# Kernel tuning notes

Hardware: AMD Instinct MI355X
Metric: run time of the kernel (lower is better)

Reference implementation:

```python
import jax, jax.numpy as jnp
import numpy as np

B, D, H, W = 32, 256, 32, 32
K = 1024
BETA = 0.25


def setup_inputs() -> dict:
    key = jax.random.key(0)
    k1, k2 = jax.random.split(key)
    z_e = jax.random.normal(k1, (B, D, H, W), dtype=jnp.float32)
    codebook_weight = jax.random.normal(k2, (K, D), dtype=jnp.float32)
    return {"z_e": z_e, "codebook_weight": codebook_weight}


def reference(z_e, codebook_weight):
    # NCHW -> NHWC, flatten to tokens [N, D]
    z_perm = jnp.transpose(z_e, (0, 2, 3, 1))            # [B, H, W, D]
    z_flat = z_perm.reshape(-1, codebook_weight.shape[1])  # [N, D]

    # Squared Euclidean distances (argmin-equivalent to torch.cdist argmin)
    # d2[n, k] = ||z_n||^2 - 2 z_n . c_k + ||c_k||^2
    d2 = (jnp.sum(z_flat * z_flat, axis=1, keepdims=True)
          - 2.0 * (z_flat @ codebook_weight.T)
          + jnp.sum(codebook_weight * codebook_weight, axis=1)[None, :])  # [N, K]
    codebook_idx = jnp.argmin(d2, axis=1)                 # [N]

    # one-hot @ codebook == gather
    z_quant = codebook_weight[codebook_idx].reshape(z_perm.shape)  # [B,H,W,D]

    # straight-through estimator, back to NCHW
    z_q = z_perm + jax.lax.stop_gradient(z_quant - z_perm)
    z_q = jnp.transpose(z_q, (0, 3, 1, 2))                # [B, D, H, W]

    loss_codebook = jnp.mean((z_quant - jax.lax.stop_gradient(z_perm)) ** 2)
    loss_commit = jnp.mean((jax.lax.stop_gradient(z_quant) - z_perm) ** 2)
    loss_vq = loss_codebook + loss_commit * BETA

    return z_q, codebook_idx[:, None], loss_vq
```

## Files before the change

### kernel.cpp

```cpp
#include <hip/hip_runtime.h>
#include <hip/hip_bf16.h>
#include <cstdint>

#define B_ 32
#define D_ 256
#define K_ 1024
#define N_TOK 32768
#define Z_ELEMS 8388608
#define OUT_IDX_OFF Z_ELEMS
#define OUT_LOSS_OFF (Z_ELEMS + N_TOK)

#define WS_CNORM_OFF 0
#define WS_PART_OFF  4096
#define WS_CBF_OFF   8192
#define WS_TOP2_OFF  532480

#define MARGIN 1.25f

typedef __attribute__((ext_vector_type(8))) short short8v;
typedef __attribute__((ext_vector_type(4))) float f32x4;
typedef unsigned long long u64;

__device__ __forceinline__ unsigned short f2bf(float x) {
    unsigned u = __float_as_uint(x);
    return (unsigned short)((u + 0x7fffu + ((u >> 16) & 1u)) >> 16);
}
__device__ __forceinline__ unsigned packf(float f) {
    unsigned u = __float_as_uint(f);
    return (u & 0x80000000u) ? ~u : (u | 0x80000000u);
}
__device__ __forceinline__ float unpackf(unsigned p) {
    unsigned u = (p & 0x80000000u) ? (p & 0x7fffffffu) : ~p;
    return __uint_as_float(u);
}

__global__ __launch_bounds__(256)
void prep_kernel(const float* __restrict__ cb, float* __restrict__ cnorm,
                 unsigned char* __restrict__ cbf) {
    const int t = threadIdx.x;
    const int blk = blockIdx.x;
    {
        int k = blk * 64 + (t >> 2);
        int part = t & 3;
        const float4* row = reinterpret_cast<const float4*>(cb + k * D_);
        float s = 0.f;
#pragma unroll
        for (int j = 0; j < 16; ++j) {
            float4 v = row[part * 16 + j];
            s += v.x * v.x + v.y * v.y + v.z * v.z + v.w * v.w;
        }
        s += __shfl_xor(s, 1);
        s += __shfl_xor(s, 2);
        if (part == 0) cnorm[k] = s;
    }
#pragma unroll
    for (int w = 0; w < 8; ++w) {
        int g = blk * 2048 + w * 256 + t;
        int lane = g & 63, ct = (g >> 6) & 7, kc = (g >> 9) & 7, cblk = g >> 12;
        int code = cblk * 128 + ct * 16 + (lane & 15);
        int d0 = kc * 32 + (lane >> 4) * 8;
        const float* src = cb + code * 256 + d0;
        float4 a = *reinterpret_cast<const float4*>(src);
        float4 b2 = *reinterpret_cast<const float4*>(src + 4);
        uint4 pk;
        pk.x = (unsigned)f2bf(a.x) | ((unsigned)f2bf(a.y) << 16);
        pk.y = (unsigned)f2bf(a.z) | ((unsigned)f2bf(a.w) << 16);
        pk.z = (unsigned)f2bf(b2.x) | ((unsigned)f2bf(b2.y) << 16);
        pk.w = (unsigned)f2bf(b2.z) | ((unsigned)f2bf(b2.w) << 16);
        *reinterpret_cast<uint4*>(cbf + (size_t)g * 16) = pk;
    }
}

__global__ __launch_bounds__(256, 2)
void screen_kernel(const float* __restrict__ z, const unsigned char* __restrict__ cbf,
                   const float* __restrict__ cnorm, unsigned* __restrict__ top2) {
    __shared__ __align__(16) unsigned char zfB[32768];
    __shared__ float cns[1024];

    const int t = threadIdx.x;
    const int lane = t & 63;
    const int wv = t >> 6;
    const int blk = blockIdx.x;
    const int b = blk >> 4;
    const int hw0 = (blk & 15) << 6;
    const float* zb = z + ((size_t)b << 18) + hw0;

    for (int i = t; i < 1024; i += 256) cns[i] = cnorm[i];

    {
        const int stok = t & 63;
        const int sh = t >> 6;
        const int tt = stok >> 4;
#pragma unroll
        for (int uu = 0; uu < 8; ++uu) {
            int u = uu * 4 + sh;
            int d0 = u * 8;
            float v[8];
#pragma unroll
            for (int j = 0; j < 8; ++j) v[j] = zb[(size_t)(d0 + j) * 1024 + stok];
            uint4 pk;
            pk.x = (unsigned)f2bf(v[0]) | ((unsigned)f2bf(v[1]) << 16);
            pk.y = (unsigned)f2bf(v[2]) | ((unsigned)f2bf(v[3]) << 16);
            pk.z = (unsigned)f2bf(v[4]) | ((unsigned)f2bf(v[5]) << 16);
            pk.w = (unsigned)f2bf(v[6]) | ((unsigned)f2bf(v[7]) << 16);
            int slot = ((u & 3) << 4) | (stok & 15);
            *reinterpret_cast<uint4*>(zfB + tt * 8192 + (u >> 2) * 1024 + slot * 16) = pk;
        }
    }
    __syncthreads();

    const unsigned char* zrd = zfB + wv * 8192 + lane * 16;
    const int rbase = (lane >> 4) << 2;

    for (int cblk = 0; cblk < 8; ++cblk) {
        f32x4 acc[8];
#pragma unroll
        for (int mt = 0; mt < 8; ++mt) acc[mt] = (f32x4){0.f, 0.f, 0.f, 0.f};
        const unsigned char* abase = cbf + (size_t)cblk * 65536 + lane * 16;
#pragma unroll
        for (int kc = 0; kc < 8; ++kc) {
            short8v bfv = *reinterpret_cast<const short8v*>(zrd + kc * 1024);
#pragma unroll
            for (int mt = 0; mt < 8; ++mt) {
                short8v af = *reinterpret_cast<const short8v*>(abase + (kc * 8 + mt) * 1024);
                acc[mt] = __builtin_amdgcn_mfma_f32_16x16x32_bf16(af, bfv, acc[mt], 0, 0, 0);
            }
        }
        unsigned k1 = 0xFFFFFFFFu, k2 = 0xFFFFFFFFu;
#pragma unroll
        for (int mt = 0; mt < 8; ++mt) {
#pragma unroll
            for (int r = 0; r < 4; ++r) {
                int code = cblk * 128 + mt * 16 + rbase + r;
                float d2a = fmaf(-2.0f, acc[mt][r], cns[code]);
                unsigned key = (packf(d2a) & 0xFFFFFC00u) | (unsigned)code;
                if (key < k1) { k2 = k1; k1 = key; }
                else if (key < k2) { k2 = key; }
            }
        }
#pragma unroll
        for (int x = 16; x <= 32; x <<= 1) {
            unsigned o1 = __shfl_xor(k1, x);
            unsigned o2 = __shfl_xor(k2, x);
            unsigned n1, n2;
            if (k1 < o1) { n1 = k1; n2 = (k2 < o1) ? k2 : o1; }
            else         { n1 = o1; n2 = (o2 < k1) ? o2 : k1; }
            k1 = n1; k2 = n2;
        }
        if (lane < 16) {
            int token = blk * 64 + wv * 16 + lane;
            *reinterpret_cast<uint2*>(top2 + ((size_t)cblk * N_TOK + token) * 2) =
                make_uint2(k1, k2);
        }
    }
}

__global__ __launch_bounds__(256)
void refgather_kernel(const float* __restrict__ z, const float* __restrict__ cb,
                      const float* __restrict__ cnorm, const unsigned* __restrict__ top2,
                      float* __restrict__ out, float* __restrict__ partials) {
    __shared__ float zsm[32][261];
    __shared__ float crows[32][257];
    __shared__ int cand[32][16];
    __shared__ int cnt[32];
    __shared__ u64 bestk[32];
    __shared__ int sidx[32];
    __shared__ float red[256];
    __shared__ int maxc;

    const int t = threadIdx.x;
    const int bh = blockIdx.x;
    const int b = bh >> 5, h = bh & 31;
    const int n0 = b * 1024 + h * 32;
    const int w = t & 31, dg = t >> 5;

    {
        const float* zp = z + ((size_t)b << 18) + h * 32 + w;
#pragma unroll
        for (int i = 0; i < 32; ++i) {
            int d = dg * 32 + i;
            zsm[w][d] = zp[(size_t)d * 1024];
        }
    }
    if (t < 32) cnt[t] = 0;
    if (t == 0) maxc = 0;
    __syncthreads();

    const int tk = t >> 3, l8 = t & 7;
    {
        uint2 kk = *reinterpret_cast<const uint2*>(
            top2 + ((size_t)l8 * N_TOK + (n0 + tk)) * 2);
        unsigned mn = kk.x;
#pragma unroll
        for (int x = 1; x < 8; x <<= 1) {
            unsigned o = __shfl_xor(mn, x);
            if (o < mn) mn = o;
        }
        float thr = unpackf(mn & 0xFFFFFC00u) + MARGIN;
        float da = unpackf(kk.x & 0xFFFFFC00u);
        if (da <= thr) { int p = atomicAdd(&cnt[tk], 1); cand[tk][p] = (int)(kk.x & 1023u); }
        float db = unpackf(kk.y & 0xFFFFFC00u);
        if (db <= thr) { int p = atomicAdd(&cnt[tk], 1); cand[tk][p] = (int)(kk.y & 1023u); }
    }
    __syncthreads();
    if (t < 32) atomicMax(&maxc, cnt[t]);
    __syncthreads();

    const int mc = maxc;
    u64 best = ~0ull;
    for (int ci = 0; ci < mc; ++ci) {
        if (ci < cnt[tk]) {
            int k = cand[tk][ci];
            const float* crow = cb + (size_t)k * 256;
            float s = 0.f;
#pragma unroll
            for (int j = 0; j < 32; ++j) {
                int d = j * 8 + l8;
                s = fmaf(zsm[tk][d], crow[d], s);
            }
#pragma unroll
            for (int x = 1; x < 8; x <<= 1) s += __shfl_xor(s, x);
            float d2 = cnorm[k] - 2.f * s;
            u64 key = ((u64)packf(d2) << 32) | (unsigned)k;
            if (key < best) best = key;
        }
    }
    if (l8 == 0) bestk[tk] = best;
    __syncthreads();
    if (t < 32) {
        int k = (int)(bestk[t] & 1023ull);
        sidx[t] = k;
        out[OUT_IDX_OFF + n0 + t] = (float)k;
    }
    __syncthreads();
    {
        const int r = t & 31, q = t >> 5;
        const float4* src = reinterpret_cast<const float4*>(cb + (size_t)sidx[r] * 256 + q * 32);
#pragma unroll
        for (int j = 0; j < 8; ++j) {
            float4 v = src[j];
            int d = q * 32 + j * 4;
            crows[r][d] = v.x; crows[r][d + 1] = v.y;
            crows[r][d + 2] = v.z; crows[r][d + 3] = v.w;
        }
    }
    __syncthreads();
    float accl = 0.f;
    float* orow = out + ((size_t)b << 18) + h * 32 + w;
#pragma unroll
    for (int i = 0; i < 32; ++i) {
        const int d = dg * 32 + i;
        const float cv = crows[w][d];
        const float zv = zsm[w][d];
        orow[(size_t)d * 1024] = cv;
        const float df = cv - zv;
        accl += df * df;
    }
    red[t] = accl;
    __syncthreads();
    for (int s = 128; s > 0; s >>= 1) {
        if (t < s) red[t] += red[t + s];
        __syncthreads();
    }
    if (t == 0) partials[bh] = red[0];
}

__global__ __launch_bounds__(256) void loss_kernel(const float* __restrict__ partials,
                                                   float* __restrict__ out) {
    __shared__ float red[256];
    const int t = threadIdx.x;
    float s = partials[t] + partials[t + 256] + partials[t + 512] + partials[t + 768];
    red[t] = s;
    __syncthreads();
    for (int st = 128; st > 0; st >>= 1) {
        if (t < st) red[t] += red[t + st];
        __syncthreads();
    }
    if (t == 0) out[OUT_LOSS_OFF] = red[0] * (1.25f / (float)Z_ELEMS);
}

extern "C" void kernel_launch(void* const* d_in, const int* in_sizes, int n_in,
                              void* d_out, int out_size, void* d_ws, size_t ws_size,
                              hipStream_t stream) {
    const float* z = (const float*)d_in[0];
    const float* cb = (const float*)d_in[1];
    float* out = (float*)d_out;
    float* cnorm = (float*)((char*)d_ws + WS_CNORM_OFF);
    float* partials = (float*)((char*)d_ws + WS_PART_OFF);
    unsigned char* cbf = (unsigned char*)d_ws + WS_CBF_OFF;
    unsigned* top2 = (unsigned*)((char*)d_ws + WS_TOP2_OFF);

    prep_kernel<<<16, 256, 0, stream>>>(cb, cnorm, cbf);
    screen_kernel<<<512, 256, 0, stream>>>(z, cbf, cnorm, top2);
    refgather_kernel<<<1024, 256, 0, stream>>>(z, cb, cnorm, top2, out, partials);
    loss_kernel<<<1, 256, 0, stream>>>(partials, out);
}
```

Before: 79.17 us.

## Split codebook blocks across waves and reuse codebook fragments over four token tiles

Each wave previously handled 16 tokens against all 8 codebook blocks, so every wave re-read the full bf16 codebook from global memory. Now each wave owns 2 codebook blocks and computes all 64 tokens of the block, so each codebook fragment load feeds 4 MFMAs. This cuts global codebook traffic per block by a factor of four. In exchange the accumulator array grows to 32 f32x4 (128 VGPRs), which may raise register pressure under launch_bounds(256,2), and the shared-memory layout of z is rearranged to match.

Result: faster. 70.78 us (-10.6%).

```diff
diff --git a/kernel.cpp b/kernel.cpp
--- a/kernel.cpp
+++ b/kernel.cpp
@@ -88,69 +88,85 @@
     for (int i = t; i < 1024; i += 256) cns[i] = cnorm[i];
 
     {
-        const int stok = t & 63;
-        const int sh = t >> 6;
-        const int tt = stok >> 4;
-#pragma unroll
-        for (int uu = 0; uu < 8; ++uu) {
-            int u = uu * 4 + sh;
-            int d0 = u * 8;
+        const int tok = t & 63;
+        const int dseg = t >> 6;
+#pragma unroll
+        for (int u = 0; u < 8; ++u) {
+            int d0 = dseg * 64 + u * 8;
             float v[8];
 #pragma unroll
-            for (int j = 0; j < 8; ++j) v[j] = zb[(size_t)(d0 + j) * 1024 + stok];
+            for (int j = 0; j < 8; ++j) v[j] = zb[(size_t)(d0 + j) * 1024 + tok];
             uint4 pk;
             pk.x = (unsigned)f2bf(v[0]) | ((unsigned)f2bf(v[1]) << 16);
             pk.y = (unsigned)f2bf(v[2]) | ((unsigned)f2bf(v[3]) << 16);
             pk.z = (unsigned)f2bf(v[4]) | ((unsigned)f2bf(v[5]) << 16);
             pk.w = (unsigned)f2bf(v[6]) | ((unsigned)f2bf(v[7]) << 16);
-            int slot = ((u & 3) << 4) | (stok & 15);
-            *reinterpret_cast<uint4*>(zfB + tt * 8192 + (u >> 2) * 1024 + slot * 16) = pk;
-        }
-    }
-    __syncthreads();
-
-    const unsigned char* zrd = zfB + wv * 8192 + lane * 16;
+            int kc = d0 >> 5;
+            int slot = (kc * 4 + (tok >> 4)) * 64 + (u & 3) * 16 + (tok & 15);
+            *reinterpret_cast<uint4*>(zfB + slot * 16) = pk;
+        }
+    }
+    __syncthreads();
+
     const int rbase = (lane >> 4) << 2;
 
-    for (int cblk = 0; cblk < 8; ++cblk) {
-        f32x4 acc[8];
-#pragma unroll
-        for (int mt = 0; mt < 8; ++mt) acc[mt] = (f32x4){0.f, 0.f, 0.f, 0.f};
+#pragma unroll
+    for (int cb2 = 0; cb2 < 2; ++cb2) {
+        const int cblk = wv * 2 + cb2;
         const unsigned char* abase = cbf + (size_t)cblk * 65536 + lane * 16;
+
+        f32x4 acc[8][4];
+#pragma unroll
+        for (int mt = 0; mt < 8; ++mt)
+#pragma unroll
+            for (int nt = 0; nt < 4; ++nt) acc[mt][nt] = (f32x4){0.f, 0.f, 0.f, 0.f};
+
 #pragma unroll
         for (int kc = 0; kc < 8; ++kc) {
-            short8v bfv = *reinterpret_cast<const short8v*>(zrd + kc * 1024);
+            short8v bfv[4];
+#pragma unroll
+            for (int nt = 0; nt < 4; ++nt)
+                bfv[nt] = *reinterpret_cast<const short8v*>(zfB + (kc * 4 + nt) * 1024 + lane * 16);
+            short8v af[8];
+#pragma unroll
+            for (int mt = 0; mt < 8; ++mt)
+                af[mt] = *reinterpret_cast<const short8v*>(abase + (kc * 8 + mt) * 1024);
+#pragma unroll
+            for (int mt = 0; mt < 8; ++mt)
+#pragma unroll
+                for (int nt = 0; nt < 4; ++nt)
+                    acc[mt][nt] = __builtin_amdgcn_mfma_f32_16x16x32_bf16(
+                        af[mt], bfv[nt], acc[mt][nt], 0, 0, 0);
+        }
+
+#pragma unroll
+        for (int nt = 0; nt < 4; ++nt) {
+            unsigned k1 = 0xFFFFFFFFu, k2 = 0xFFFFFFFFu;
 #pragma unroll
             for (int mt = 0; mt < 8; ++mt) {
-                short8v af = *reinterpret_cast<const short8v*>(abase + (kc * 8 + mt) * 1024);
-                acc[mt] = __builtin_amdgcn_mfma_f32_16x16x32_bf16(af, bfv, acc[mt], 0, 0, 0);
+#pragma unroll
+                for (int r = 0; r < 4; ++r) {
+                    int code = cblk * 128 + mt * 16 + rbase + r;
+                    float d2a = fmaf(-2.0f, acc[mt][nt][r], cns[code]);
+                    unsigned key = (packf(d2a) & 0xFFFFFC00u) | (unsigned)code;
+                    if (key < k1) { k2 = k1; k1 = key; }
+                    else if (key < k2) { k2 = key; }
+                }
             }
-        }
-        unsigned k1 = 0xFFFFFFFFu, k2 = 0xFFFFFFFFu;
-#pragma unroll
-        for (int mt = 0; mt < 8; ++mt) {
-#pragma unroll
-            for (int r = 0; r < 4; ++r) {
-                int code = cblk * 128 + mt * 16 + rbase + r;
-                float d2a = fmaf(-2.0f, acc[mt][r], cns[code]);
-                unsigned key = (packf(d2a) & 0xFFFFFC00u) | (unsigned)code;
-                if (key < k1) { k2 = k1; k1 = key; }
-                else if (key < k2) { k2 = key; }
+#pragma unroll
+            for (int x = 16; x <= 32; x <<= 1) {
+                unsigned o1 = __shfl_xor(k1, x);
+                unsigned o2 = __shfl_xor(k2, x);
+                unsigned n1, n2;
+                if (k1 < o1) { n1 = k1; n2 = (k2 < o1) ? k2 : o1; }
+                else         { n1 = o1; n2 = (o2 < k1) ? o2 : k1; }
+                k1 = n1; k2 = n2;
             }
-        }
-#pragma unroll
-        for (int x = 16; x <= 32; x <<= 1) {
-            unsigned o1 = __shfl_xor(k1, x);
-            unsigned o2 = __shfl_xor(k2, x);
-            unsigned n1, n2;
-            if (k1 < o1) { n1 = k1; n2 = (k2 < o1) ? k2 : o1; }
-            else         { n1 = o1; n2 = (o2 < k1) ? o2 : k1; }
-            k1 = n1; k2 = n2;
-        }
-        if (lane < 16) {
-            int token = blk * 64 + wv * 16 + lane;
-            *reinterpret_cast<uint2*>(top2 + ((size_t)cblk * N_TOK + token) * 2) =
-                make_uint2(k1, k2);
+            if (lane < 16) {
+                int token = blk * 64 + nt * 16 + lane;
+                *reinterpret_cast<uint2*>(top2 + ((size_t)cblk * N_TOK + token) * 2) =
+                    make_uint2(k1, k2);
+            }
         }
     }
 }
```

## Stage codebook tiles through double-buffered LDS with register prefetch in screen GEMM

Applied to the files above, without the earlier changes.

The screening GEMM used to have each wave read codebook bf16 fragments straight from global memory. Now the block cooperatively prefetches the next 8KB codebook slice into registers and stores it into a double-buffered LDS region. Every wave then reads the A fragments from LDS, with one __syncthreads per k-chunk. This removes redundant global/L2 traffic across the four waves, but it adds 64 block barriers and 16KB more LDS, and it drops the occupancy hint of 2 blocks per CU.

New measurement: 75.22 us. -5.0%, faster.

```diff
diff --git a/kernel.cpp b/kernel.cpp
--- a/kernel.cpp
+++ b/kernel.cpp
@@ -71,10 +71,11 @@
     }
 }
 
-__global__ __launch_bounds__(256, 2)
-void screen_kernel(const float* __restrict__ z, const unsigned char* __restrict__ cbf,
-                   const float* __restrict__ cnorm, unsigned* __restrict__ top2) {
+__global__ __launch_bounds__(256)
+void mm_kernel(const float* __restrict__ z, const unsigned char* __restrict__ cbf,
+               const float* __restrict__ cnorm, unsigned* __restrict__ top2) {
     __shared__ __align__(16) unsigned char zfB[32768];
+    __shared__ __align__(16) unsigned char Abuf[16384];
     __shared__ float cns[1024];
 
     const int t = threadIdx.x;
@@ -84,73 +85,95 @@
     const int b = blk >> 4;
     const int hw0 = (blk & 15) << 6;
     const float* zb = z + ((size_t)b << 18) + hw0;
+    const uint4* cbf4 = reinterpret_cast<const uint4*>(cbf);
+
+    uint4 c0a = cbf4[t];
+    uint4 c0b = cbf4[256 + t];
 
     for (int i = t; i < 1024; i += 256) cns[i] = cnorm[i];
 
     {
-        const int stok = t & 63;
-        const int sh = t >> 6;
-        const int tt = stok >> 4;
-#pragma unroll
-        for (int uu = 0; uu < 8; ++uu) {
-            int u = uu * 4 + sh;
-            int d0 = u * 8;
+        const int tok = t & 63;
+        const int dseg = t >> 6;
+#pragma unroll
+        for (int u = 0; u < 8; ++u) {
+            int d0 = dseg * 64 + u * 8;
             float v[8];
 #pragma unroll
-            for (int j = 0; j < 8; ++j) v[j] = zb[(size_t)(d0 + j) * 1024 + stok];
+            for (int j = 0; j < 8; ++j) v[j] = zb[(size_t)(d0 + j) * 1024 + tok];
             uint4 pk;
             pk.x = (unsigned)f2bf(v[0]) | ((unsigned)f2bf(v[1]) << 16);
             pk.y = (unsigned)f2bf(v[2]) | ((unsigned)f2bf(v[3]) << 16);
             pk.z = (unsigned)f2bf(v[4]) | ((unsigned)f2bf(v[5]) << 16);
             pk.w = (unsigned)f2bf(v[6]) | ((unsigned)f2bf(v[7]) << 16);
-            int slot = ((u & 3) << 4) | (stok & 15);
-            *reinterpret_cast<uint4*>(zfB + tt * 8192 + (u >> 2) * 1024 + slot * 16) = pk;
-        }
-    }
-    __syncthreads();
-
-    const unsigned char* zrd = zfB + wv * 8192 + lane * 16;
+            int kc = d0 >> 5;
+            *reinterpret_cast<uint4*>(zfB + (kc * 4 + (tok >> 4)) * 1024 +
+                                      ((u & 3) * 16 + (tok & 15)) * 16) = pk;
+        }
+    }
+    {
+        uint4* d = reinterpret_cast<uint4*>(Abuf);
+        d[t] = c0a;
+        d[256 + t] = c0b;
+    }
+    __syncthreads();
+
     const int rbase = (lane >> 4) << 2;
 
     for (int cblk = 0; cblk < 8; ++cblk) {
         f32x4 acc[8];
 #pragma unroll
         for (int mt = 0; mt < 8; ++mt) acc[mt] = (f32x4){0.f, 0.f, 0.f, 0.f};
-        const unsigned char* abase = cbf + (size_t)cblk * 65536 + lane * 16;
-#pragma unroll
+
         for (int kc = 0; kc < 8; ++kc) {
-            short8v bfv = *reinterpret_cast<const short8v*>(zrd + kc * 1024);
+            const int s = cblk * 8 + kc;
+            uint4 na, nb;
+            if (s < 63) {
+                na = cbf4[(size_t)(s + 1) * 512 + t];
+                nb = cbf4[(size_t)(s + 1) * 512 + 256 + t];
+            }
+            const unsigned char* ab = Abuf + (s & 1) * 8192 + lane * 16;
+            short8v bfv = *reinterpret_cast<const short8v*>(
+                zfB + (kc * 4 + wv) * 1024 + lane * 16);
 #pragma unroll
             for (int mt = 0; mt < 8; ++mt) {
-                short8v af = *reinterpret_cast<const short8v*>(abase + (kc * 8 + mt) * 1024);
+                short8v af = *reinterpret_cast<const short8v*>(ab + mt * 1024);
                 acc[mt] = __builtin_amdgcn_mfma_f32_16x16x32_bf16(af, bfv, acc[mt], 0, 0, 0);
             }
-        }
-        unsigned k1 = 0xFFFFFFFFu, k2 = 0xFFFFFFFFu;
-#pragma unroll
-        for (int mt = 0; mt < 8; ++mt) {
-#pragma unroll
-            for (int r = 0; r < 4; ++r) {
-                int code = cblk * 128 + mt * 16 + rbase + r;
-                float d2a = fmaf(-2.0f, acc[mt][r], cns[code]);
-                unsigned key = (packf(d2a) & 0xFFFFFC00u) | (unsigned)code;
-                if (key < k1) { k2 = k1; k1 = key; }
-                else if (key < k2) { k2 = key; }
-            }
-        }
-#pragma unroll
-        for (int x = 16; x <= 32; x <<= 1) {
-            unsigned o1 = __shfl_xor(k1, x);
-            unsigned o2 = __shfl_xor(k2, x);
-            unsigned n1, n2;
-            if (k1 < o1) { n1 = k1; n2 = (k2 < o1) ? k2 : o1; }
-            else         { n1 = o1; n2 = (o2 < k1) ? o2 : k1; }
-            k1 = n1; k2 = n2;
-        }
-        if (lane < 16) {
-            int token = blk * 64 + wv * 16 + lane;
-            *reinterpret_cast<uint2*>(top2 + ((size_t)cblk * N_TOK + token) * 2) =
-                make_uint2(k1, k2);
+            if (kc == 7) {
+                unsigned k1 = 0xFFFFFFFFu, k2 = 0xFFFFFFFFu;
+#pragma unroll
+                for (int mt = 0; mt < 8; ++mt) {
+#pragma unroll
+                    for (int r = 0; r < 4; ++r) {
+                        int code = cblk * 128 + mt * 16 + rbase + r;
+                        float d2a = fmaf(-2.0f, acc[mt][r], cns[code]);
+                        unsigned key = (packf(d2a) & 0xFFFFFC00u) | (unsigned)code;
+                        if (key < k1) { k2 = k1; k1 = key; }
+                        else if (key < k2) { k2 = key; }
+                    }
+                }
+#pragma unroll
+                for (int x = 16; x <= 32; x <<= 1) {
+                    unsigned o1 = __shfl_xor(k1, x);
+                    unsigned o2 = __shfl_xor(k2, x);
+                    unsigned n1, n2;
+                    if (k1 < o1) { n1 = k1; n2 = (k2 < o1) ? k2 : o1; }
+                    else         { n1 = o1; n2 = (o2 < k1) ? o2 : k1; }
+                    k1 = n1; k2 = n2;
+                }
+                if (lane < 16) {
+                    int token = blk * 64 + wv * 16 + lane;
+                    *reinterpret_cast<uint2*>(top2 + ((size_t)cblk * N_TOK + token) * 2) =
+                        make_uint2(k1, k2);
+                }
+            }
+            if (s < 63) {
+                uint4* d = reinterpret_cast<uint4*>(Abuf + ((s + 1) & 1) * 8192);
+                d[t] = na;
+                d[256 + t] = nb;
+            }
+            __syncthreads();
         }
     }
 }
@@ -291,7 +314,7 @@
     unsigned* top2 = (unsigned*)((char*)d_ws + WS_TOP2_OFF);
 
     prep_kernel<<<16, 256, 0, stream>>>(cb, cnorm, cbf);
-    screen_kernel<<<512, 256, 0, stream>>>(z, cbf, cnorm, top2);
+    mm_kernel<<<512, 256, 0, stream>>>(z, cbf, cnorm, top2);
     refgather_kernel<<<1024, 256, 0, stream>>>(z, cb, cnorm, top2, out, partials);
     loss_kernel<<<1, 256, 0, stream>>>(partials, out);
 }
```

## Split screen GEMM across 8 waves with 2x2 code/token tiling per wave

Applied to the files above, without the earlier changes.

The screening GEMM kernel now runs 512 threads per block instead of 256. Each wave covers two token tiles and two of the eight codebook blocks, rather than 16 tokens against all eight blocks. Each codebook fragment loaded from global memory now feeds two MFMAs, which halves per-wave global codebook traffic and shortens each wave's serial loop. The cost is a doubled accumulator register footprint and the removed launch_bounds occupancy hint, which may reduce resident blocks per CU.

Result: faster. 69.95 us (-11.7%).

```diff
diff --git a/kernel.cpp b/kernel.cpp
--- a/kernel.cpp
+++ b/kernel.cpp
@@ -71,86 +71,100 @@
     }
 }
 
-__global__ __launch_bounds__(256, 2)
-void screen_kernel(const float* __restrict__ z, const unsigned char* __restrict__ cbf,
-                   const float* __restrict__ cnorm, unsigned* __restrict__ top2) {
+__global__
+void mm_kernel(const float* __restrict__ z, const unsigned char* __restrict__ cbf,
+               const float* __restrict__ cnorm, unsigned* __restrict__ top2) {
     __shared__ __align__(16) unsigned char zfB[32768];
     __shared__ float cns[1024];
 
     const int t = threadIdx.x;
     const int lane = t & 63;
     const int wv = t >> 6;
+    const int th = wv & 1;
+    const int cq = wv >> 1;
     const int blk = blockIdx.x;
     const int b = blk >> 4;
     const int hw0 = (blk & 15) << 6;
     const float* zb = z + ((size_t)b << 18) + hw0;
 
-    for (int i = t; i < 1024; i += 256) cns[i] = cnorm[i];
-
-    {
-        const int stok = t & 63;
-        const int sh = t >> 6;
-        const int tt = stok >> 4;
-#pragma unroll
-        for (int uu = 0; uu < 8; ++uu) {
-            int u = uu * 4 + sh;
-            int d0 = u * 8;
+    if (t < 512) { cns[t] = cnorm[t]; cns[512 + t] = cnorm[512 + t]; }
+
+    {
+        const int tok = t & 63;
+        const int kc = t >> 6;
+#pragma unroll
+        for (int u = 0; u < 4; ++u) {
+            int d0 = kc * 32 + u * 8;
             float v[8];
 #pragma unroll
-            for (int j = 0; j < 8; ++j) v[j] = zb[(size_t)(d0 + j) * 1024 + stok];
+            for (int j = 0; j < 8; ++j) v[j] = zb[(size_t)(d0 + j) * 1024 + tok];
             uint4 pk;
             pk.x = (unsigned)f2bf(v[0]) | ((unsigned)f2bf(v[1]) << 16);
             pk.y = (unsigned)f2bf(v[2]) | ((unsigned)f2bf(v[3]) << 16);
             pk.z = (unsigned)f2bf(v[4]) | ((unsigned)f2bf(v[5]) << 16);
             pk.w = (unsigned)f2bf(v[6]) | ((unsigned)f2bf(v[7]) << 16);
-            int slot = ((u & 3) << 4) | (stok & 15);
-            *reinterpret_cast<uint4*>(zfB + tt * 8192 + (u >> 2) * 1024 + slot * 16) = pk;
-        }
-    }
-    __syncthreads();
-
-    const unsigned char* zrd = zfB + wv * 8192 + lane * 16;
+            *reinterpret_cast<uint4*>(zfB + (kc * 4 + (tok >> 4)) * 1024 +
+                                      (u * 16 + (tok & 15)) * 16) = pk;
+        }
+    }
+    __syncthreads();
+
     const int rbase = (lane >> 4) << 2;
-
-    for (int cblk = 0; cblk < 8; ++cblk) {
-        f32x4 acc[8];
-#pragma unroll
-        for (int mt = 0; mt < 8; ++mt) acc[mt] = (f32x4){0.f, 0.f, 0.f, 0.f};
+    const unsigned char* zrd0 = zfB + (th * 2 + 0) * 1024 + lane * 16;
+    const unsigned char* zrd1 = zfB + (th * 2 + 1) * 1024 + lane * 16;
+
+#pragma unroll
+    for (int cb2 = 0; cb2 < 2; ++cb2) {
+        const int cblk = cq * 2 + cb2;
         const unsigned char* abase = cbf + (size_t)cblk * 65536 + lane * 16;
+
+        f32x4 acc[8][2];
+#pragma unroll
+        for (int mt = 0; mt < 8; ++mt) {
+            acc[mt][0] = (f32x4){0.f, 0.f, 0.f, 0.f};
+            acc[mt][1] = (f32x4){0.f, 0.f, 0.f, 0.f};
+        }
+
 #pragma unroll
         for (int kc = 0; kc < 8; ++kc) {
-            short8v bfv = *reinterpret_cast<const short8v*>(zrd + kc * 1024);
+            short8v bf0 = *reinterpret_cast<const short8v*>(zrd0 + kc * 4096);
+            short8v bf1 = *reinterpret_cast<const short8v*>(zrd1 + kc * 4096);
 #pragma unroll
             for (int mt = 0; mt < 8; ++mt) {
                 short8v af = *reinterpret_cast<const short8v*>(abase + (kc * 8 + mt) * 1024);
-                acc[mt] = __builtin_amdgcn_mfma_f32_16x16x32_bf16(af, bfv, acc[mt], 0, 0, 0);
-            }
-        }
-        unsigned k1 = 0xFFFFFFFFu, k2 = 0xFFFFFFFFu;
-#pragma unroll
-        for (int mt = 0; mt < 8; ++mt) {
-#pragma unroll
-            for (int r = 0; r < 4; ++r) {
-                int code = cblk * 128 + mt * 16 + rbase + r;
-                float d2a = fmaf(-2.0f, acc[mt][r], cns[code]);
-                unsigned key = (packf(d2a) & 0xFFFFFC00u) | (unsigned)code;
-                if (key < k1) { k2 = k1; k1 = key; }
-                else if (key < k2) { k2 = key; }
-            }
-        }
-#pragma unroll
-        for (int x = 16; x <= 32; x <<= 1) {
-            unsigned o1 = __shfl_xor(k1, x);
-            unsigned o2 = __shfl_xor(k2, x);
-            unsigned n1, n2;
-            if (k1 < o1) { n1 = k1; n2 = (k2 < o1) ? k2 : o1; }
-            else         { n1 = o1; n2 = (o2 < k1) ? o2 : k1; }
-            k1 = n1; k2 = n2;
-        }
-        if (lane < 16) {
-            int token = blk * 64 + wv * 16 + lane;
-            *reinterpret_cast<uint2*>(top2 + ((size_t)cblk * N_TOK + token) * 2) =
-                make_uint2(k1, k2);
+                acc[mt][0] = __builtin_amdgcn_mfma_f32_16x16x32_bf16(af, bf0, acc[mt][0], 0, 0, 0);
+                acc[mt][1] = __builtin_amdgcn_mfma_f32_16x16x32_bf16(af, bf1, acc[mt][1], 0, 0, 0);
+            }
+        }
+
+#pragma unroll
+        for (int nt = 0; nt < 2; ++nt) {
+            unsigned k1 = 0xFFFFFFFFu, k2 = 0xFFFFFFFFu;
+#pragma unroll
+            for (int mt = 0; mt < 8; ++mt) {
+#pragma unroll
+                for (int r = 0; r < 4; ++r) {
+                    int code = cblk * 128 + mt * 16 + rbase + r;
+                    float d2a = fmaf(-2.0f, acc[mt][nt][r], cns[code]);
+                    unsigned key = (packf(d2a) & 0xFFFFFC00u) | (unsigned)code;
+                    if (key < k1) { k2 = k1; k1 = key; }
+                    else if (key < k2) { k2 = key; }
+                }
+            }
+#pragma unroll
+            for (int x = 16; x <= 32; x <<= 1) {
+                unsigned o1 = __shfl_xor(k1, x);
+                unsigned o2 = __shfl_xor(k2, x);
+                unsigned n1, n2;
+                if (k1 < o1) { n1 = k1; n2 = (k2 < o1) ? k2 : o1; }
+                else         { n1 = o1; n2 = (o2 < k1) ? o2 : k1; }
+                k1 = n1; k2 = n2;
+            }
+            if (lane < 16) {
+                int token = blk * 64 + th * 32 + nt * 16 + lane;
+                *reinterpret_cast<uint2*>(top2 + ((size_t)cblk * N_TOK + token) * 2) =
+                    make_uint2(k1, k2);
+            }
         }
     }
 }
@@ -291,7 +305,7 @@
     unsigned* top2 = (unsigned*)((char*)d_ws + WS_TOP2_OFF);
 
     prep_kernel<<<16, 256, 0, stream>>>(cb, cnorm, cbf);
-    screen_kernel<<<512, 256, 0, stream>>>(z, cbf, cnorm, top2);
+    mm_kernel<<<512, 512, 0, stream>>>(z, cbf, cnorm, top2);
     refgather_kernel<<<1024, 256, 0, stream>>>(z, cb, cnorm, top2, out, partials);
     loss_kernel<<<1, 256, 0, stream>>>(partials, out);
 }
```
